# Performance work log

Hardware: AMD Instinct MI355X
Metric: run time of the kernel (lower is better)

## Reference

```python
import jax, jax.numpy as jnp
import numpy as np

NBINS = 256


def setup_inputs() -> dict:
    key = jax.random.key(0)
    x = jax.random.uniform(key, (16, 3, 1024, 1024), dtype=jnp.float32)
    return {"x": x}


def reference(x):
    b, c, h, w = x.shape
    n = b * c
    xf = x.reshape(n, h * w)                      # (n, N) per-channel rows

    # global min/max over the whole tensor (matches torch.histogram range)
    mn = xf.min()
    mx = xf.max()
    span = mx - mn

    # per-row histogram via scatter-add; last bin is right-closed like torch.histogram
    scale = NBINS / span
    idx = jnp.clip(jnp.floor((xf - mn) * scale).astype(jnp.int32), 0, NBINS - 1)
    flat_idx = (jnp.arange(n, dtype=jnp.int32)[:, None] * NBINS + idx).reshape(-1)
    hist = jax.ops.segment_sum(
        jnp.ones((n * h * w,), dtype=jnp.float32), flat_idx,
        num_segments=n * NBINS,
    ).reshape(n, NBINS)
    hist = hist / hist.sum(axis=1, keepdims=True)  # normalized histograms

    # vectorized Otsu: cumulative weights/means -> inter-class variance
    t = jnp.arange(NBINS, dtype=hist.dtype)
    w_bg = jnp.cumsum(hist, axis=1)               # background weight up to t
    s_bg = jnp.cumsum(hist * t, axis=1)           # background weighted sum
    total = s_bg[:, -1:]                          # sum_i i*hist[i]
    w_fg = 1.0 - w_bg
    valid = (w_bg > 0) & (w_fg > 0)
    mean_bg = s_bg / jnp.where(w_bg > 0, w_bg, 1.0)
    mean_fg = (total - s_bg) / jnpp_safe(w_fg) if False else (total - s_bg) / jnp.where(w_fg > 0, w_fg, 1.0)
    var = jnp.where(valid, w_bg * w_fg * (mean_bg - mean_fg) ** 2, -jnp.inf)
    t_opt = jnp.argmax(var, axis=1)               # first max, like strict `>` loop

    # threshold = right edge of the optimal bin
    edges = mn + span * (jnp.arange(NBINS + 1, dtype=x.dtype) / NBINS)
    thresh = edges[t_opt + 1]                     # (n,)

    out = jnp.where(xf <= thresh[:, None], jnp.zeros((), x.dtype), xf)
    return out.reshape(b, c, h, w)
```

## Files before the change

### kernel.cpp

```cpp
#include <hip/hip_runtime.h>
#include <stdint.h>

#define NBINS 256
#define HW_SHIFT 20
#define HW4_SHIFT (HW_SHIFT-2)
#define BLK_PER_IMG 64
#define NCOPY 32

typedef float nfloat4 __attribute__((ext_vector_type(4)));

__device__ __forceinline__ unsigned enc_f(float f) {
    unsigned u = __float_as_uint(f);
    return u ^ ((unsigned)((int)u >> 31) | 0x80000000u);
}
__device__ __forceinline__ float dec_f(unsigned e) {
    unsigned u = (e & 0x80000000u) ? (e ^ 0x80000000u) : ~e;
    return __uint_as_float(u);
}

__global__ void k_init(unsigned* mmo, unsigned* hist, int nhist) {
    int t = threadIdx.x + blockIdx.x * blockDim.x;
    if (t == 0) { mmo[0] = 0xFFFFFFFFu; mmo[1] = 0u; }
    for (int i = t; i < nhist; i += blockDim.x * gridDim.x) hist[i] = 0u;
}

__global__ void k_minmax(const float4* __restrict__ x, unsigned* mmo, long n4) {
    unsigned mn = 0xFFFFFFFFu, mx = 0u;
    long stride = (long)gridDim.x * blockDim.x;
    for (long i = (long)blockIdx.x * blockDim.x + threadIdx.x; i < n4; i += stride) {
        float4 v = x[i];
        unsigned e0 = enc_f(v.x), e1 = enc_f(v.y), e2 = enc_f(v.z), e3 = enc_f(v.w);
        mn = min(mn, min(min(e0, e1), min(e2, e3)));
        mx = max(mx, max(max(e0, e1), max(e2, e3)));
    }
    for (int off = 32; off > 0; off >>= 1) {
        mn = min(mn, (unsigned)__shfl_down((int)mn, off));
        mx = max(mx, (unsigned)__shfl_down((int)mx, off));
    }
    __shared__ unsigned smn[4], smx[4];
    int lane = threadIdx.x & 63, w = threadIdx.x >> 6;
    if (lane == 0) { smn[w] = mn; smx[w] = mx; }
    __syncthreads();
    if (threadIdx.x == 0) {
        for (int j = 1; j < (int)(blockDim.x >> 6); j++) {
            mn = min(mn, smn[j]); mx = max(mx, smx[j]);
        }
        atomicMin(&mmo[0], mn);
        atomicMax(&mmo[1], mx);
    }
}

__global__ void k_hist(const float4* __restrict__ x, const unsigned* __restrict__ mmo,
                       unsigned* __restrict__ ghist) {
    __shared__ unsigned sh[NBINS * NCOPY];
    for (int i = threadIdx.x; i < NBINS * NCOPY; i += blockDim.x) sh[i] = 0u;
    __syncthreads();
    float mn = dec_f(mmo[0]);
    float mx = dec_f(mmo[1]);
    float span = mx - mn;
    float scale = __fdiv_rn(256.0f, span);
    int img = blockIdx.x / BLK_PER_IMG;
    int blk = blockIdx.x % BLK_PER_IMG;
    const float4* base = x + ((long)img << HW4_SHIFT);
    const int n4i = 1 << HW4_SHIFT;
    int c = threadIdx.x & (NCOPY - 1);
    for (int i = blk * blockDim.x + threadIdx.x; i < n4i; i += BLK_PER_IMG * blockDim.x) {
        float4 v = base[i];
        int b0 = (int)floorf((v.x - mn) * scale);
        int b1 = (int)floorf((v.y - mn) * scale);
        int b2 = (int)floorf((v.z - mn) * scale);
        int b3 = (int)floorf((v.w - mn) * scale);
        b0 = min(max(b0, 0), NBINS - 1);
        b1 = min(max(b1, 0), NBINS - 1);
        b2 = min(max(b2, 0), NBINS - 1);
        b3 = min(max(b3, 0), NBINS - 1);
        atomicAdd(&sh[b0 * NCOPY + c], 1u);
        atomicAdd(&sh[b1 * NCOPY + c], 1u);
        atomicAdd(&sh[b2 * NCOPY + c], 1u);
        atomicAdd(&sh[b3 * NCOPY + c], 1u);
    }
    __syncthreads();
    int bin = threadIdx.x;
    unsigned sum = 0;
    #pragma unroll
    for (int k = 0; k < NCOPY; k++) {
        int cc = (k + threadIdx.x) & (NCOPY - 1);
        sum += sh[bin * NCOPY + cc];
    }
    if (sum) atomicAdd(&ghist[img * NBINS + bin], sum);
}

__global__ void k_otsu(const unsigned* __restrict__ ghist, const unsigned* __restrict__ mmo,
                       float* __restrict__ thresh, int nimg) {
    __shared__ unsigned sh[48 * (NBINS + 1)];
    int total_h = nimg * NBINS;
    for (int i = threadIdx.x; i < total_h; i += blockDim.x) {
        int im = i >> 8, b = i & 255;
        sh[im * (NBINS + 1) + b] = ghist[i];
    }
    __syncthreads();
    int i = threadIdx.x;
    if (i >= nimg) return;
    const unsigned* h = sh + i * (NBINS + 1);
    const float inv_total = 1.0f / 1048576.0f;
    float w = 0.0f, s = 0.0f;
    for (int t = 0; t < NBINS; t++) {
        float p = __fmul_rn((float)h[t], inv_total);
        w = __fadd_rn(w, p);
        s = __fadd_rn(s, __fmul_rn(p, (float)t));
    }
    float total = s;
    float best = -__builtin_inff();
    int bestt = 0;
    w = 0.0f; s = 0.0f;
    for (int t = 0; t < NBINS; t++) {
        float p = __fmul_rn((float)h[t], inv_total);
        w = __fadd_rn(w, p);
        s = __fadd_rn(s, __fmul_rn(p, (float)t));
        float wf = __fsub_rn(1.0f, w);
        float var;
        if (w > 0.0f && wf > 0.0f) {
            float mb = __fdiv_rn(s, w);
            float mf = __fdiv_rn(__fsub_rn(total, s), wf);
            float d = __fsub_rn(mb, mf);
            var = __fmul_rn(__fmul_rn(w, wf), __fmul_rn(d, d));
        } else {
            var = -__builtin_inff();
        }
        if (var > best) { best = var; bestt = t; }
    }
    float mn = dec_f(mmo[0]);
    float mx = dec_f(mmo[1]);
    float span = __fsub_rn(mx, mn);
    float q = __fmul_rn((float)(bestt + 1), 1.0f / 256.0f);
    thresh[i] = __fadd_rn(mn, __fmul_rn(span, q));
}

__global__ void k_apply(const float4* __restrict__ x, nfloat4* __restrict__ out,
                        const float* __restrict__ thresh, long n4) {
    long stride = (long)gridDim.x * blockDim.x;
    for (long i = (long)blockIdx.x * blockDim.x + threadIdx.x; i < n4; i += stride) {
        int img = (int)(i >> HW4_SHIFT);
        float th = thresh[img];
        float4 v = x[i];
        nfloat4 o;
        o.x = (v.x <= th) ? 0.0f : v.x;
        o.y = (v.y <= th) ? 0.0f : v.y;
        o.z = (v.z <= th) ? 0.0f : v.z;
        o.w = (v.w <= th) ? 0.0f : v.w;
        __builtin_nontemporal_store(o, &out[i]);
    }
}

extern "C" void kernel_launch(void* const* d_in, const int* in_sizes, int n_in,
                              void* d_out, int out_size, void* d_ws, size_t ws_size,
                              hipStream_t stream) {
    const float* x = (const float*)d_in[0];
    float* out = (float*)d_out;
    long n = (long)in_sizes[0];
    long n4 = n >> 2;
    int nimg = (int)(n >> HW_SHIFT);

    unsigned* mmo = (unsigned*)d_ws;
    unsigned* ghist = mmo + 2;
    float* thresh = (float*)(ghist + nimg * NBINS);

    k_init<<<48, 256, 0, stream>>>(mmo, ghist, nimg * NBINS);
    k_minmax<<<2048, 256, 0, stream>>>((const float4*)x, mmo, n4);
    k_hist<<<nimg * BLK_PER_IMG, 256, 0, stream>>>((const float4*)x, mmo, ghist);
    k_otsu<<<1, 256, 0, stream>>>(ghist, mmo, thresh, nimg);
    k_apply<<<4096, 256, 0, stream>>>((const float4*)x, (nfloat4*)out, thresh, n4);
}
```

Measured before the change: 476.7 us.

## Replace global atomics with per-block partials and parallelize Otsu per image

Removes the init kernel and global atomics: min/max blocks write per-block partials reduced by a new single-block kernel, and histogram blocks write per-block partial histograms summed in the Otsu kernel. Otsu now runs one block per image instead of one thread per image in a single block. The histogram uses half as many blocks per image, each reading a contiguous chunk, and min/max uses fewer blocks. This trades an extra launch and more workspace for fewer atomics and more parallel Otsu, at the risk of lower occupancy in the histogram stage.

```diff
diff --git a/kernel.cpp b/kernel.cpp
--- a/kernel.cpp
+++ b/kernel.cpp
@@ -4,8 +4,9 @@
 #define NBINS 256
 #define HW_SHIFT 20
 #define HW4_SHIFT (HW_SHIFT-2)
-#define BLK_PER_IMG 64
+#define BLK_PER_IMG 32
 #define NCOPY 32
+#define MM_BLOCKS 1024
 
 typedef float nfloat4 __attribute__((ext_vector_type(4)));
 
@@ -18,13 +19,8 @@
     return __uint_as_float(u);
 }
 
-__global__ void k_init(unsigned* mmo, unsigned* hist, int nhist) {
-    int t = threadIdx.x + blockIdx.x * blockDim.x;
-    if (t == 0) { mmo[0] = 0xFFFFFFFFu; mmo[1] = 0u; }
-    for (int i = t; i < nhist; i += blockDim.x * gridDim.x) hist[i] = 0u;
-}
 
-__global__ void k_minmax(const float4* __restrict__ x, unsigned* mmo, long n4) {
+__global__ void k_minmax(const float4* __restrict__ x, unsigned* __restrict__ bmm, long n4) {
     unsigned mn = 0xFFFFFFFFu, mx = 0u;
     long stride = (long)gridDim.x * blockDim.x;
     for (long i = (long)blockIdx.x * blockDim.x + threadIdx.x; i < n4; i += stride) {
@@ -45,13 +41,35 @@
         for (int j = 1; j < (int)(blockDim.x >> 6); j++) {
             mn = min(mn, smn[j]); mx = max(mx, smx[j]);
         }
-        atomicMin(&mmo[0], mn);
-        atomicMax(&mmo[1], mx);
+        bmm[2 * blockIdx.x]     = mn;
+        bmm[2 * blockIdx.x + 1] = mx;
+    }
+}
+
+__global__ void k_reduce(const unsigned* __restrict__ bmm, unsigned* __restrict__ mmo) {
+    unsigned mn = 0xFFFFFFFFu, mx = 0u;
+    for (int i = threadIdx.x; i < MM_BLOCKS; i += blockDim.x) {
+        mn = min(mn, bmm[2 * i]);
+        mx = max(mx, bmm[2 * i + 1]);
+    }
+    for (int off = 32; off > 0; off >>= 1) {
+        mn = min(mn, (unsigned)__shfl_down((int)mn, off));
+        mx = max(mx, (unsigned)__shfl_down((int)mx, off));
+    }
+    __shared__ unsigned smn[4], smx[4];
+    int lane = threadIdx.x & 63, w = threadIdx.x >> 6;
+    if (lane == 0) { smn[w] = mn; smx[w] = mx; }
+    __syncthreads();
+    if (threadIdx.x == 0) {
+        for (int j = 1; j < (int)(blockDim.x >> 6); j++) {
+            mn = min(mn, smn[j]); mx = max(mx, smx[j]);
+        }
+        mmo[0] = mn; mmo[1] = mx;
     }
 }
 
 __global__ void k_hist(const float4* __restrict__ x, const unsigned* __restrict__ mmo,
-                       unsigned* __restrict__ ghist) {
+                       unsigned* __restrict__ partial) {
     __shared__ unsigned sh[NBINS * NCOPY];
     for (int i = threadIdx.x; i < NBINS * NCOPY; i += blockDim.x) sh[i] = 0u;
     __syncthreads();
@@ -61,10 +79,10 @@
     float scale = __fdiv_rn(256.0f, span);
     int img = blockIdx.x / BLK_PER_IMG;
     int blk = blockIdx.x % BLK_PER_IMG;
-    const float4* base = x + ((long)img << HW4_SHIFT);
-    const int n4i = 1 << HW4_SHIFT;
+    const int chunk = (1 << HW4_SHIFT) / BLK_PER_IMG;
+    const float4* base = x + ((long)img << HW4_SHIFT) + (long)blk * chunk;
     int c = threadIdx.x & (NCOPY - 1);
-    for (int i = blk * blockDim.x + threadIdx.x; i < n4i; i += BLK_PER_IMG * blockDim.x) {
+    for (int i = threadIdx.x; i < chunk; i += blockDim.x) {
         float4 v = base[i];
         int b0 = (int)floorf((v.x - mn) * scale);
         int b1 = (int)floorf((v.y - mn) * scale);
@@ -87,36 +105,36 @@
         int cc = (k + threadIdx.x) & (NCOPY - 1);
         sum += sh[bin * NCOPY + cc];
     }
-    if (sum) atomicAdd(&ghist[img * NBINS + bin], sum);
+    partial[(long)blockIdx.x * NBINS + bin] = sum;
 }
 
-__global__ void k_otsu(const unsigned* __restrict__ ghist, const unsigned* __restrict__ mmo,
-                       float* __restrict__ thresh, int nimg) {
-    __shared__ unsigned sh[48 * (NBINS + 1)];
-    int total_h = nimg * NBINS;
-    for (int i = threadIdx.x; i < total_h; i += blockDim.x) {
-        int im = i >> 8, b = i & 255;
-        sh[im * (NBINS + 1) + b] = ghist[i];
-    }
+__global__ void k_otsu(const unsigned* __restrict__ partial, const unsigned* __restrict__ mmo,
+                       float* __restrict__ thresh) {
+    __shared__ unsigned h[NBINS];
+    int img = blockIdx.x;
+    int bin = threadIdx.x;
+    const unsigned* p = partial + (long)img * BLK_PER_IMG * NBINS;
+    unsigned sum = 0;
+    #pragma unroll
+    for (int k = 0; k < BLK_PER_IMG; k++) sum += p[k * NBINS + bin];
+    h[bin] = sum;
     __syncthreads();
-    int i = threadIdx.x;
-    if (i >= nimg) return;
-    const unsigned* h = sh + i * (NBINS + 1);
+    if (threadIdx.x != 0) return;
     const float inv_total = 1.0f / 1048576.0f;
     float w = 0.0f, s = 0.0f;
     for (int t = 0; t < NBINS; t++) {
-        float p = __fmul_rn((float)h[t], inv_total);
-        w = __fadd_rn(w, p);
-        s = __fadd_rn(s, __fmul_rn(p, (float)t));
+        float pp = __fmul_rn((float)h[t], inv_total);
+        w = __fadd_rn(w, pp);
+        s = __fadd_rn(s, __fmul_rn(pp, (float)t));
     }
     float total = s;
     float best = -__builtin_inff();
     int bestt = 0;
     w = 0.0f; s = 0.0f;
     for (int t = 0; t < NBINS; t++) {
-        float p = __fmul_rn((float)h[t], inv_total);
-        w = __fadd_rn(w, p);
-        s = __fadd_rn(s, __fmul_rn(p, (float)t));
+        float pp = __fmul_rn((float)h[t], inv_total);
+        w = __fadd_rn(w, pp);
+        s = __fadd_rn(s, __fmul_rn(pp, (float)t));
         float wf = __fsub_rn(1.0f, w);
         float var;
         if (w > 0.0f && wf > 0.0f) {
@@ -133,7 +151,7 @@
     float mx = dec_f(mmo[1]);
     float span = __fsub_rn(mx, mn);
     float q = __fmul_rn((float)(bestt + 1), 1.0f / 256.0f);
-    thresh[i] = __fadd_rn(mn, __fmul_rn(span, q));
+    thresh[img] = __fadd_rn(mn, __fmul_rn(span, q));
 }
 
 __global__ void k_apply(const float4* __restrict__ x, nfloat4* __restrict__ out,
@@ -161,13 +179,14 @@
     long n4 = n >> 2;
     int nimg = (int)(n >> HW_SHIFT);
 
-    unsigned* mmo = (unsigned*)d_ws;
-    unsigned* ghist = mmo + 2;
-    float* thresh = (float*)(ghist + nimg * NBINS);
+    unsigned* bmm = (unsigned*)d_ws;
+    unsigned* mmo = bmm + 2 * MM_BLOCKS;
+    unsigned* partial = mmo + 2;
+    float* thresh = (float*)(partial + (long)nimg * BLK_PER_IMG * NBINS);
 
-    k_init<<<48, 256, 0, stream>>>(mmo, ghist, nimg * NBINS);
-    k_minmax<<<2048, 256, 0, stream>>>((const float4*)x, mmo, n4);
-    k_hist<<<nimg * BLK_PER_IMG, 256, 0, stream>>>((const float4*)x, mmo, ghist);
-    k_otsu<<<1, 256, 0, stream>>>(ghist, mmo, thresh, nimg);
+    k_minmax<<<MM_BLOCKS, 256, 0, stream>>>((const float4*)x, bmm, n4);
+    k_reduce<<<1, 256, 0, stream>>>(bmm, mmo);
+    k_hist<<<nimg * BLK_PER_IMG, 256, 0, stream>>>((const float4*)x, mmo, partial);
+    k_otsu<<<nimg, 256, 0, stream>>>(partial, mmo, thresh);
     k_apply<<<4096, 256, 0, stream>>>((const float4*)x, (nfloat4*)out, thresh, n4);
 }
```

After: 439.8 us. 7.7% less time.
